# Kernel tuning notes

Measured on AMD Instinct MI355X. Metric: run time of the kernel, lower is better.

## Reference

```python
import jax, jax.numpy as jnp
import numpy as np


def _ste_sign(x):
    # sign with straight-through (identity) gradient, matching gradient_override_map({'Sign': 'Identity'})
    return x + jax.lax.stop_gradient(jnp.sign(x) - x)


def _ternarize(W):
    # threshold = 0.7 * mean(|W|)
    t = 0.7 * jnp.mean(jnp.abs(W))
    # alpha = mean of |W| over entries with |W| strictly beyond threshold
    pos = jnp.where(W > t, W, jnp.zeros_like(W))
    neg = jnp.where(W < -t, W, jnp.zeros_like(W))
    a = jnp.abs(pos + neg)
    n = jnp.sum(jnp.where(a > 0, jnp.ones_like(a), jnp.zeros_like(a)))
    alpha = jnp.sum(a) / n
    # ternary weights in {-1, 0, +1}: sign(sign(W+t) + sign(W-t))
    Wq = _ste_sign(_ste_sign(W + t) + _ste_sign(W - t))
    return alpha * Wq


def setup_inputs() -> dict:
    key = jax.random.key(0)
    kx, kw = jax.random.split(key)
    x = jax.random.normal(kx, (32, 56, 56, 256), dtype=jnp.float32)      # NHWC
    W = jax.random.normal(kw, (3, 3, 256, 256), dtype=jnp.float32) * 0.02  # HWIO, stddev=0.02 init
    b = jnp.zeros((256,), dtype=jnp.float32)
    return {"x": x, "W": W, "b": b}


def reference(x, W, b):
    Wq = _ternarize(W)
    y = jax.lax.conv_general_dilated(
        x, Wq,
        window_strides=(1, 1),
        padding='SAME',
        dimension_numbers=('NHWC', 'HWIO', 'NHWC'),
    )
    return y + b  # act = identity
```

## Files before the change

kernel.cpp:

```cpp
#include <hip/hip_runtime.h>
#include <hip/hip_bf16.h>
#include <stdint.h>


typedef __attribute__((ext_vector_type(8))) short short8;
typedef __attribute__((ext_vector_type(4))) float floatx4;

#define NW_ELEMS 589824
#define K_TOTAL 2304
#define PR_OFF 0
#define QV_OFF 2560
#define QC_OFF 5120
#define WQT_OFF 8192
#define RED_BLOCKS 288

__device__ __forceinline__ void async16(const void* g, void* l) {
  __builtin_amdgcn_global_load_lds(
      (const __attribute__((address_space(1))) void*)g,
      (__attribute__((address_space(3))) void*)l, 16, 0, 0);
}

__device__ __forceinline__ ushort f2bf(float f) {
  __hip_bfloat16 h = __float2bfloat16(f);
  return *reinterpret_cast<ushort*>(&h);
}

__global__ __launch_bounds__(256) void sumabs_kernel(
    const float* __restrict__ W, double* __restrict__ pr) {
  __shared__ double sds[4];
  double v = 0.0;
#pragma unroll
  for (int j = 0; j < 8; j++) {
    uint i = (blockIdx.x * 8 + j) * 256 + threadIdx.x;
    v += (double)fabsf(W[i]);
  }
#pragma unroll
  for (int off = 32; off; off >>= 1) v += __shfl_down(v, off);
  if ((threadIdx.x & 63) == 0) sds[threadIdx.x >> 6] = v;
  __syncthreads();
  if (threadIdx.x == 0) pr[blockIdx.x] = sds[0] + sds[1] + sds[2] + sds[3];
}

__global__ __launch_bounds__(256) void quant_kernel(
    const float* __restrict__ W, ushort* __restrict__ WqT,
    const double* __restrict__ pr, double* __restrict__ qv,
    unsigned long long* __restrict__ qc) {
  __shared__ double sds[4];
  __shared__ unsigned long long cds[4];
  double p = pr[threadIdx.x];
  if (threadIdx.x < 32) p += pr[256 + threadIdx.x];
#pragma unroll
  for (int off = 32; off; off >>= 1) p += __shfl_down(p, off);
  if ((threadIdx.x & 63) == 0) sds[threadIdx.x >> 6] = p;
  __syncthreads();
  double s = sds[0] + sds[1] + sds[2] + sds[3];
  float t = (float)(0.7 * (s / (double)NW_ELEMS));
  __syncthreads();

  double v = 0.0;
  unsigned long long cnt = 0;
  ushort u[8];
#pragma unroll
  for (int j = 0; j < 8; j++) {
    uint i = (blockIdx.x * 8 + j) * 256 + threadIdx.x;
    float w = W[i];
    bool pos = (w > t), neg = (w < -t);
    u[j] = pos ? (ushort)0x3F80 : (neg ? (ushort)0xBF80 : (ushort)0);
    if (pos || neg) { v += (double)fabsf(w); cnt++; }
  }
  *(uint4*)(WqT + (size_t)threadIdx.x * K_TOTAL + blockIdx.x * 8) = *(uint4*)u;
#pragma unroll
  for (int off = 32; off; off >>= 1) {
    v += __shfl_down(v, off);
    cnt += __shfl_down(cnt, off);
  }
  if ((threadIdx.x & 63) == 0) { sds[threadIdx.x >> 6] = v; cds[threadIdx.x >> 6] = cnt; }
  __syncthreads();
  if (threadIdx.x == 0) {
    qv[blockIdx.x] = sds[0] + sds[1] + sds[2] + sds[3];
    qc[blockIdx.x] = cds[0] + cds[1] + cds[2] + cds[3];
  }
}

__global__ __launch_bounds__(256, 2) void conv_kernel(
    const float* __restrict__ x, const ushort* __restrict__ WqT,
    const double* __restrict__ qv, const unsigned long long* __restrict__ qc,
    const float* __restrict__ bias, float* __restrict__ out) {
  __shared__ __attribute__((aligned(16))) ushort Alds[128 * 64];
  __shared__ __attribute__((aligned(16))) ushort Blds[128 * 64];
  __shared__ double ads[4];
  __shared__ double acs[4];
  uint tid = threadIdx.x;
  uint bm = blockIdx.x >> 1, bn = blockIdx.x & 1;

  uint chunk = tid & 7;
  uint rbase = tid >> 3;
  uint ceff = chunk ^ (rbase & 7);
  int hh[4], ww[4];
  int abase[4];
  const ushort* bsrc[4];
#pragma unroll
  for (int i = 0; i < 4; i++) {
    uint row = i * 32 + rbase;
    uint gm = bm * 128 + row;
    uint n = gm / 3136;
    uint rem = gm - n * 3136;
    uint h = rem / 56;
    uint w = rem - h * 56;
    hh[i] = (int)h;
    ww[i] = (int)w;
    abase[i] = (((int)n * 56 + (int)h - 1) * 56 + (int)w - 1) * 256 + (int)(ceff * 8);
    bsrc[i] = WqT + ((size_t)(bn * 128 + row) * K_TOTAL + ceff * 8);
  }

  floatx4 acc[4][4];
#pragma unroll
  for (int mt = 0; mt < 4; mt++)
#pragma unroll
    for (int nt = 0; nt < 4; nt++) acc[mt][nt] = (floatx4){0.f, 0.f, 0.f, 0.f};

  uint lane = tid & 63;
  uint wv = tid >> 6;
  uint wm = wv >> 1, wn = wv & 1;
  uint fr = lane & 15, fq = lane >> 4;
  uint a_row = (wm * 64 + fr) * 128;
  uint b_row = (wn * 64 + fr) * 128;
  uint swz = (fr & 7) * 16;

  for (int ks = 0; ks < 36; ks++) {
    uint kcq = (uint)ks / 9;
    uint tap = (uint)ks - kcq * 9;
    int ky = (int)(tap / 3);
    int kx = (int)(tap - ky * 3);
    int aoffe = (ky * 56 + kx) * 256 + (int)(kcq * 64);
    uint boffe = tap * 256 + kcq * 64;

    __syncthreads();
#pragma unroll
    for (int i = 0; i < 4; i++)
      async16(bsrc[i] + boffe, (char*)Blds + i * 4096 + tid * 16);
#pragma unroll
    for (int i = 0; i < 4; i++) {
      int ih = hh[i] + ky - 1;
      int iw = ww[i] + kx - 1;
      bool valid = ((uint)ih < 56u) && ((uint)iw < 56u);
      float4 f0 = {0.f, 0.f, 0.f, 0.f}, f1 = {0.f, 0.f, 0.f, 0.f};
      if (valid) {
        const float* p = x + (abase[i] + aoffe);
        f0 = *(const float4*)p;
        f1 = *(const float4*)(p + 4);
      }
      ushort u[8];
      u[0] = f2bf(f0.x); u[1] = f2bf(f0.y); u[2] = f2bf(f0.z); u[3] = f2bf(f0.w);
      u[4] = f2bf(f1.x); u[5] = f2bf(f1.y); u[6] = f2bf(f1.z); u[7] = f2bf(f1.w);
      *(uint4*)((char*)Alds + i * 4096 + tid * 16) = *(uint4*)u;
    }
    __syncthreads();

#pragma unroll
    for (int kk = 0; kk < 2; kk++) {
      uint csl = ((uint)(kk * 64) + fq * 16) ^ swz;
      short8 af[4], bfr[4];
#pragma unroll
      for (int mt = 0; mt < 4; mt++)
        af[mt] = *(const short8*)((const char*)Alds + a_row + mt * 2048 + csl);
#pragma unroll
      for (int nt = 0; nt < 4; nt++)
        bfr[nt] = *(const short8*)((const char*)Blds + b_row + nt * 2048 + csl);
#pragma unroll
      for (int mt = 0; mt < 4; mt++)
#pragma unroll
        for (int nt = 0; nt < 4; nt++)
          acc[mt][nt] = __builtin_amdgcn_mfma_f32_16x16x32_bf16(
              af[mt], bfr[nt], acc[mt][nt], 0, 0, 0);
    }
  }

  double av = qv[tid];
  double ac = (double)qc[tid];
  if (tid < 32) { av += qv[256 + tid]; ac += (double)qc[256 + tid]; }
#pragma unroll
  for (int off = 32; off; off >>= 1) {
    av += __shfl_down(av, off);
    ac += __shfl_down(ac, off);
  }
  if ((tid & 63) == 0) { ads[tid >> 6] = av; acs[tid >> 6] = ac; }
  __syncthreads();
  float alpha = (float)((ads[0] + ads[1] + ads[2] + ads[3]) /
                        (acs[0] + acs[1] + acs[2] + acs[3]));

#pragma unroll
  for (int mt = 0; mt < 4; mt++) {
    uint mb = bm * 128 + wm * 64 + mt * 16 + fq * 4;
#pragma unroll
    for (int r = 0; r < 4; r++) {
      float* orow = out + (size_t)(mb + r) * 256;
#pragma unroll
      for (int nt = 0; nt < 4; nt++) {
        uint n = bn * 128 + wn * 64 + nt * 16 + fr;
        orow[n] = acc[mt][nt][r] * alpha + bias[n];
      }
    }
  }
}

extern "C" void kernel_launch(void* const* d_in, const int* in_sizes, int n_in,
                              void* d_out, int out_size, void* d_ws, size_t ws_size,
                              hipStream_t stream) {
  const float* x = (const float*)d_in[0];
  const float* W = (const float*)d_in[1];
  const float* b = (const float*)d_in[2];
  float* out = (float*)d_out;

  double* pr = (double*)((char*)d_ws + PR_OFF);
  double* qv = (double*)((char*)d_ws + QV_OFF);
  unsigned long long* qc = (unsigned long long*)((char*)d_ws + QC_OFF);
  ushort* WqT = (ushort*)((char*)d_ws + WQT_OFF);

  sumabs_kernel<<<RED_BLOCKS, 256, 0, stream>>>(W, pr);
  quant_kernel<<<RED_BLOCKS, 256, 0, stream>>>(W, WqT, pr, qv, qc);
  conv_kernel<<<1568, 256, 0, stream>>>(x, WqT, qv, qc, b, out);
}
```

Measured before the change: 342.6 us.

## Double-buffer LDS tiles and prefetch next K-step input into registers

```diff
diff --git a/kernel.cpp b/kernel.cpp
--- a/kernel.cpp
+++ b/kernel.cpp
@@ -86,8 +86,8 @@
     const float* __restrict__ x, const ushort* __restrict__ WqT,
     const double* __restrict__ qv, const unsigned long long* __restrict__ qc,
     const float* __restrict__ bias, float* __restrict__ out) {
-  __shared__ __attribute__((aligned(16))) ushort Alds[128 * 64];
-  __shared__ __attribute__((aligned(16))) ushort Blds[128 * 64];
+  __shared__ __attribute__((aligned(16))) ushort Alds[2][128 * 64];
+  __shared__ __attribute__((aligned(16))) ushort Blds[2][128 * 64];
   __shared__ double ads[4];
   __shared__ double acs[4];
   uint tid = threadIdx.x;
@@ -127,35 +127,67 @@
   uint b_row = (wn * 64 + fr) * 128;
   uint swz = (fr & 7) * 16;
 
+  float4 pf0[4], pf1[4];
+  {
+#pragma unroll
+    for (int i = 0; i < 4; i++) {
+      int ih = hh[i] - 1, iw = ww[i] - 1;
+      bool valid = ((uint)ih < 56u) && ((uint)iw < 56u);
+      pf0[i] = (float4){0.f, 0.f, 0.f, 0.f};
+      pf1[i] = (float4){0.f, 0.f, 0.f, 0.f};
+      if (valid) {
+        const float* p = x + abase[i];
+        pf0[i] = *(const float4*)p;
+        pf1[i] = *(const float4*)(p + 4);
+      }
+    }
+#pragma unroll
+    for (int i = 0; i < 4; i++)
+      async16(bsrc[i], (char*)&Blds[0][0] + i * 4096 + tid * 16);
+  }
+
+#pragma unroll 1
   for (int ks = 0; ks < 36; ks++) {
-    uint kcq = (uint)ks / 9;
-    uint tap = (uint)ks - kcq * 9;
-    int ky = (int)(tap / 3);
-    int kx = (int)(tap - ky * 3);
-    int aoffe = (ky * 56 + kx) * 256 + (int)(kcq * 64);
-    uint boffe = tap * 256 + kcq * 64;
-
+    uint p = (uint)ks & 1;
+    char* Ab = (char*)&Alds[p][0];
+    char* Bb = (char*)&Blds[p][0];
+
+#pragma unroll
+    for (int i = 0; i < 4; i++) {
+      ushort u[8];
+      u[0] = f2bf(pf0[i].x); u[1] = f2bf(pf0[i].y);
+      u[2] = f2bf(pf0[i].z); u[3] = f2bf(pf0[i].w);
+      u[4] = f2bf(pf1[i].x); u[5] = f2bf(pf1[i].y);
+      u[6] = f2bf(pf1[i].z); u[7] = f2bf(pf1[i].w);
+      *(uint4*)(Ab + i * 4096 + tid * 16) = *(uint4*)u;
+    }
     __syncthreads();
-#pragma unroll
-    for (int i = 0; i < 4; i++)
-      async16(bsrc[i] + boffe, (char*)Blds + i * 4096 + tid * 16);
-#pragma unroll
-    for (int i = 0; i < 4; i++) {
-      int ih = hh[i] + ky - 1;
-      int iw = ww[i] + kx - 1;
-      bool valid = ((uint)ih < 56u) && ((uint)iw < 56u);
-      float4 f0 = {0.f, 0.f, 0.f, 0.f}, f1 = {0.f, 0.f, 0.f, 0.f};
-      if (valid) {
-        const float* p = x + (abase[i] + aoffe);
-        f0 = *(const float4*)p;
-        f1 = *(const float4*)(p + 4);
+
+    if (ks < 35) {
+      uint ks1 = (uint)ks + 1;
+      uint kcq = ks1 / 9;
+      uint tap = ks1 - kcq * 9;
+      int ky = (int)(tap / 3);
+      int kx = (int)(tap - ky * 3);
+      int aoffe = (ky * 56 + kx) * 256 + (int)(kcq * 64);
+      uint boffe = tap * 256 + kcq * 64;
+#pragma unroll
+      for (int i = 0; i < 4; i++) {
+        int ih = hh[i] + ky - 1;
+        int iw = ww[i] + kx - 1;
+        bool valid = ((uint)ih < 56u) && ((uint)iw < 56u);
+        pf0[i] = (float4){0.f, 0.f, 0.f, 0.f};
+        pf1[i] = (float4){0.f, 0.f, 0.f, 0.f};
+        if (valid) {
+          const float* gp = x + (abase[i] + aoffe);
+          pf0[i] = *(const float4*)gp;
+          pf1[i] = *(const float4*)(gp + 4);
+        }
       }
-      ushort u[8];
-      u[0] = f2bf(f0.x); u[1] = f2bf(f0.y); u[2] = f2bf(f0.z); u[3] = f2bf(f0.w);
-      u[4] = f2bf(f1.x); u[5] = f2bf(f1.y); u[6] = f2bf(f1.z); u[7] = f2bf(f1.w);
-      *(uint4*)((char*)Alds + i * 4096 + tid * 16) = *(uint4*)u;
-    }
-    __syncthreads();
+#pragma unroll
+      for (int i = 0; i < 4; i++)
+        async16(bsrc[i] + boffe, (char*)&Blds[p ^ 1][0] + i * 4096 + tid * 16);
+    }
 
 #pragma unroll
     for (int kk = 0; kk < 2; kk++) {
@@ -163,10 +195,10 @@
       short8 af[4], bfr[4];
 #pragma unroll
       for (int mt = 0; mt < 4; mt++)
-        af[mt] = *(const short8*)((const char*)Alds + a_row + mt * 2048 + csl);
+        af[mt] = *(const short8*)(Ab + a_row + mt * 2048 + csl);
 #pragma unroll
       for (int nt = 0; nt < 4; nt++)
-        bfr[nt] = *(const short8*)((const char*)Blds + b_row + nt * 2048 + csl);
+        bfr[nt] = *(const short8*)(Bb + b_row + nt * 2048 + csl);
 #pragma unroll
       for (int mt = 0; mt < 4; mt++)
 #pragma unroll
```

Measured after the change: 344.1 us. Within noise of the previous version (+0.4%).
